# Kernel optimization log

Measured on AMD Instinct MI355X. Metric: run time of the kernel, lower is better.

Reference implementation:

```python
import jax, jax.numpy as jnp
import numpy as np

N_CLUSTERS = 2048
MAX_ITER = 5


def setup_inputs() -> dict:
    key = jax.random.key(0)
    k1, k2 = jax.random.split(key)
    X = jax.random.normal(k1, (131072, 128), dtype=jnp.float32)
    init_centroids = jax.random.normal(k2, (N_CLUSTERS, 128), dtype=jnp.float32)
    return {"X": X, "init_centroids": init_centroids}


def _euc_sim(a, b):
    # 2 a.b^T - |a|^2 - |b|^2  (negative squared euclidean distance)
    return (2.0 * (a @ b.T)
            - jnp.sum(a * a, axis=1)[:, None]
            - jnp.sum(b * b, axis=1)[None, :])


def reference(X, init_centroids):
    K = init_centroids.shape[0]

    def step(centroids, _):
        sim = _euc_sim(X, centroids)              # [N, K]
        closest = jnp.argmax(sim, axis=-1)         # [N]
        sums = jax.ops.segment_sum(X, closest, num_segments=K)        # [K, d]
        counts = jax.ops.segment_sum(jnp.ones_like(closest, dtype=X.dtype),
                                     closest, num_segments=K)         # [K]
        # full-batch branch: c_grad = mask @ x / mask.sum(-1), NaN -> 0
        c_grad = jnp.where(counts[:, None] > 0, sums / jnp.maximum(counts, 1.0)[:, None], 0.0)
        # minibatch is None => lr = 1 => centroids <- c_grad
        return c_grad, closest

    centroids, closest_hist = jax.lax.scan(step, init_centroids, None, length=MAX_ITER)
    labels = closest_hist[-1]
    return centroids, labels
```

## Files before the change

kernel.cpp:

```cpp
#include <hip/hip_runtime.h>
#include <hip/hip_bf16.h>

#define NP 131072
#define D 128
#define KC 2048
#define ITERS 5

#define TAU 0.03f

#if defined(__has_builtin)
#if __has_builtin(__builtin_amdgcn_global_load_lds)
#define USE_GLL 1
#endif
#endif

typedef short bf16x8 __attribute__((ext_vector_type(8)));
typedef float f32x4 __attribute__((ext_vector_type(4)));

__device__ inline unsigned short f2bf(float x) {
    __hip_bfloat16 b = __float2bfloat16(x);
    return *reinterpret_cast<unsigned short*>(&b);
}
__device__ inline float bf2f(unsigned short u) {
    union { unsigned int i; float f; } c; c.i = ((unsigned int)u) << 16; return c.f;
}

__device__ inline size_t pslot(int k, int d, int hl) {
    int g = k >> 4, t15 = k & 15, ks = d >> 5, q = (d >> 3) & 3, e = d & 7;
    return ((size_t)((ks * 128 + g) * 2 + hl)) * 512 + (q * 16 + t15) * 8 + e;
}

__global__ void init_kernel(const float* __restrict__ initC,
                            double* __restrict__ C64, double* __restrict__ CT64,
                            unsigned short* __restrict__ Pn) {
    int t = blockIdx.x * 256 + threadIdx.x;
    float v = initC[t];
    C64[t] = (double)v;
    CT64[(size_t)(t & 127) * KC + (t >> 7)] = (double)v;
    unsigned short h = f2bf(v);
    int k = t >> 7, d = t & 127;
    Pn[pslot(k, d, 0)] = h;
    Pn[pslot(k, d, 1)] = f2bf(v - bf2f(h));
}

__global__ void cnorm_kernel(const double* __restrict__ C64,
                             double* __restrict__ n64, float* __restrict__ n32,
                             int* __restrict__ counter) {
    int r = blockIdx.x * 4 + (threadIdx.x >> 6);
    int lane = threadIdx.x & 63;
    double a = C64[(size_t)r * D + lane * 2];
    double b = C64[(size_t)r * D + lane * 2 + 1];
    double s = a * a + b * b;
#pragma unroll
    for (int m = 1; m < 64; m <<= 1) s += __shfl_xor(s, m, 64);
    if (lane == 0) { n64[r] = s; n32[r] = (float)s; }
    if (blockIdx.x == 0 && threadIdx.x == 0) *counter = 0;
}

__global__ __launch_bounds__(256, 4)
void assign_kernel(const float* __restrict__ X,
                   const unsigned short* __restrict__ Pn,
                   const float* __restrict__ cnorm,
                   int* __restrict__ labels,
                   int* __restrict__ list,
                   int* __restrict__ counter) {
    __shared__ __align__(16) char lds[32768];

    const int tid = threadIdx.x;
    const int lane = tid & 63;
    const int wid = tid >> 6;
    const int wrow = wid >> 1;
    const int wcol = wid & 1;
    const int t15 = lane & 15;
    const int q = lane >> 4;
    const int pbase = blockIdx.x * 64;

#pragma unroll
    for (int i = 0; i < 8; i++) {
        int f = i * 256 + tid;
        int row = f >> 5, c4 = f & 31;
        float4 v = *(const float4*)&X[(size_t)(pbase + row) * D + c4 * 4];
        unsigned short h0 = f2bf(v.x), h1 = f2bf(v.y), h2 = f2bf(v.z), h3 = f2bf(v.w);
        unsigned short l0 = f2bf(v.x - bf2f(h0)), l1 = f2bf(v.y - bf2f(h1));
        unsigned short l2 = f2bf(v.z - bf2f(h2)), l3 = f2bf(v.w - bf2f(h3));
        uint2 ph = { (unsigned)h0 | ((unsigned)h1 << 16), (unsigned)h2 | ((unsigned)h3 << 16) };
        uint2 pl = { (unsigned)l0 | ((unsigned)l1 << 16), (unsigned)l2 | ((unsigned)l3 << 16) };
        int ad = (row * 256 + c4 * 8) ^ ((row & 7) << 4);
        *(uint2*)(lds + ad) = ph;
        *(uint2*)(lds + 16384 + ad) = pl;
    }
    __syncthreads();

    bf16x8 rah[2][4], ral[2][4];
#pragma unroll
    for (int rt = 0; rt < 2; rt++) {
        int row = wrow * 32 + rt * 16 + t15;
        int sw = (row & 7) << 4;
#pragma unroll
        for (int ks = 0; ks < 4; ks++) {
            int ad = (row * 256 + ks * 64 + q * 16) ^ sw;
            rah[rt][ks] = *(const bf16x8*)(lds + ad);
            ral[rt][ks] = *(const bf16x8*)(lds + 16384 + ad);
        }
    }
    __syncthreads();

    float b1[8], b2[8];
    int i1[8];
#pragma unroll
    for (int s = 0; s < 8; s++) { b1[s] = -INFINITY; b2[s] = -INFINITY; i1[s] = 0x7fffffff; }

    const char* PnB = (const char*)Pn;

#pragma unroll
    for (int i = 0; i < 4; i++) {
        int seg = wid * 4 + i;
        const char* src = PnB + seg * 1024;
#if USE_GLL
        __builtin_amdgcn_global_load_lds(
            (const __attribute__((address_space(1))) unsigned int*)(src + lane * 16),
            (__attribute__((address_space(3))) unsigned int*)(lds + seg * 1024),
            16, 0, 0);
#else
        uint4 v = *(const uint4*)(src + lane * 16);
        *(uint4*)(lds + seg * 1024 + lane * 16) = v;
#endif
    }
    __syncthreads();

    for (int ct = 0; ct < KC / 128; ct++) {
        f32x4 acc[2][4];
#pragma unroll
        for (int rt = 0; rt < 2; rt++)
#pragma unroll
            for (int cj = 0; cj < 4; cj++) acc[rt][cj] = (f32x4){0.f, 0.f, 0.f, 0.f};

#pragma unroll
        for (int ks = 0; ks < 4; ks++) {
            const int cur = (ct * 4 + ks) & 1;
            char* bcur = lds + cur * 16384;
            char* bnext = lds + (cur ^ 1) * 16384;

            const int nct = (ks == 3) ? ((ct < 15) ? ct + 1 : 15) : ct;
            const int nks = (ks + 1) & 3;
            const char* nsrc = PnB + ((size_t)(nks * 128 + nct * 8)) * 2048;
#pragma unroll
            for (int i = 0; i < 4; i++) {
                int seg = wid * 4 + i;
#if USE_GLL
                __builtin_amdgcn_global_load_lds(
                    (const __attribute__((address_space(1))) unsigned int*)(nsrc + seg * 1024 + lane * 16),
                    (__attribute__((address_space(3))) unsigned int*)(bnext + seg * 1024),
                    16, 0, 0);
#else
                uint4 v = *(const uint4*)(nsrc + seg * 1024 + lane * 16);
                *(uint4*)(bnext + seg * 1024 + lane * 16) = v;
#endif
            }

            __builtin_amdgcn_s_setprio(1);
#pragma unroll
            for (int cj = 0; cj < 4; cj++) {
                int gl = wcol * 4 + cj;
                bf16x8 bh = *(const bf16x8*)(bcur + gl * 2048 + lane * 16);
                bf16x8 bl = *(const bf16x8*)(bcur + gl * 2048 + 1024 + lane * 16);
#pragma unroll
                for (int rt = 0; rt < 2; rt++) {
                    acc[rt][cj] = __builtin_amdgcn_mfma_f32_16x16x32_bf16(rah[rt][ks], bh, acc[rt][cj], 0, 0, 0);
                    acc[rt][cj] = __builtin_amdgcn_mfma_f32_16x16x32_bf16(rah[rt][ks], bl, acc[rt][cj], 0, 0, 0);
                    acc[rt][cj] = __builtin_amdgcn_mfma_f32_16x16x32_bf16(ral[rt][ks], bh, acc[rt][cj], 0, 0, 0);
                }
            }
            __builtin_amdgcn_s_setprio(0);
            __syncthreads();
        }

#pragma unroll
        for (int cj = 0; cj < 4; cj++) {
            int col = ct * 128 + wcol * 64 + cj * 16 + t15;
            float cnv = cnorm[col];
#pragma unroll
            for (int rt = 0; rt < 2; rt++)
#pragma unroll
                for (int rg = 0; rg < 4; rg++) {
                    int s = rt * 4 + rg;
                    float sv = __builtin_fmaf(2.0f, acc[rt][cj][rg], -cnv);
                    bool gt1 = sv > b1[s];
                    float mx2 = fmaxf(b2[s], sv);
                    b2[s] = gt1 ? b1[s] : mx2;
                    i1[s] = gt1 ? col : i1[s];
                    b1[s] = gt1 ? sv : b1[s];
                }
        }
    }

#pragma unroll
    for (int s = 0; s < 8; s++) {
#pragma unroll
        for (int m = 1; m < 16; m <<= 1) {
            float ob1 = __shfl_xor(b1[s], m, 64);
            int   oi  = __shfl_xor(i1[s], m, 64);
            float ob2 = __shfl_xor(b2[s], m, 64);
            bool gt = ob1 > b1[s];
            bool eq = ob1 == b1[s];
            float nb2 = gt ? fmaxf(b1[s], ob2) : fmaxf(b2[s], ob1);
            nb2 = eq ? b1[s] : nb2;
            int ni = gt ? oi : i1[s];
            ni = (eq && oi < i1[s]) ? oi : ni;
            b1[s] = gt ? ob1 : b1[s];
            b2[s] = nb2;
            i1[s] = ni;
        }
    }

    __syncthreads();
    float* mb1 = (float*)lds;
    float* mb2 = ((float*)lds) + 128;
    int*   mi1 = (int*)(((float*)lds) + 256);
    if (t15 == 0) {
#pragma unroll
        for (int rt = 0; rt < 2; rt++)
#pragma unroll
            for (int rg = 0; rg < 4; rg++) {
                int s = rt * 4 + rg;
                int row = wrow * 32 + rt * 16 + q * 4 + rg;
                mb1[wcol * 64 + row] = b1[s];
                mb2[wcol * 64 + row] = b2[s];
                mi1[wcol * 64 + row] = i1[s];
            }
    }
    __syncthreads();
    if (tid < 64) {
        float a1 = mb1[tid], a2 = mb2[tid];  int ai = mi1[tid];
        float c1 = mb1[64 + tid], c2 = mb2[64 + tid];  int ci = mi1[64 + tid];
        float best, second;  int bi;
        if (a1 > c1)      { best = a1; bi = ai; second = fmaxf(a2, c1); }
        else if (a1 < c1) { best = c1; bi = ci; second = fmaxf(c2, a1); }
        else              { best = a1; bi = (ai < ci) ? ai : ci; second = a1; }
        int p = pbase + tid;
        labels[p] = bi;
        if (best - second < TAU) {
            int idx = atomicAdd(counter, 1);
            list[idx] = p;
        }
    }
}

__global__ void recheck_kernel(const float* __restrict__ X,
                               const double* __restrict__ CT64,
                               const double* __restrict__ cn64,
                               const int* __restrict__ list,
                               const int* __restrict__ counter,
                               int* __restrict__ labels) {
    __shared__ float xrow[D];
    __shared__ double rb[4];
    __shared__ int ri[4];
    int cnt = *counter;
    for (int ii = blockIdx.x; ii < cnt; ii += gridDim.x) {
        int p = list[ii];
        __syncthreads();
        if (threadIdx.x < D) xrow[threadIdx.x] = X[(size_t)p * D + threadIdx.x];
        __syncthreads();
        double xn = 0.0;
#pragma unroll 16
        for (int d = 0; d < D; d++) {
            double xv = (double)xrow[d];
            xn = fma(xv, xv, xn);
        }
        double best = -1.0e300;
        int bi = 0x7fffffff;
#pragma unroll
        for (int g = 0; g < 8; g++) {
            int c = threadIdx.x + 256 * g;
            double acc = 0.0;
#pragma unroll 16
            for (int d = 0; d < D; d++)
                acc = fma((double)xrow[d], CT64[(size_t)d * KC + c], acc);
            double s = 2.0 * acc - xn - cn64[c];
            if (s > best || (s == best && c < bi)) { best = s; bi = c; }
        }
#pragma unroll
        for (int m = 1; m < 64; m <<= 1) {
            double ob = __shfl_xor(best, m, 64);
            int oi = __shfl_xor(bi, m, 64);
            if (ob > best || (ob == best && oi < bi)) { best = ob; bi = oi; }
        }
        int w = threadIdx.x >> 6;
        if ((threadIdx.x & 63) == 0) { rb[w] = best; ri[w] = bi; }
        __syncthreads();
        if (threadIdx.x == 0) {
            double bb = rb[0]; int bbi = ri[0];
            for (int w2 = 1; w2 < 4; w2++)
                if (rb[w2] > bb || (rb[w2] == bb && ri[w2] < bbi)) { bb = rb[w2]; bbi = ri[w2]; }
            labels[p] = bbi;
        }
    }
}

__global__ void accum_kernel(const float* __restrict__ X,
                             const int* __restrict__ labels,
                             double* __restrict__ sums,
                             int* __restrict__ counts) {
    __shared__ double sred[4][D];
    __shared__ int cred[4];
    const int k = blockIdx.x;
    const int lane = threadIdx.x & 63;
    const int w = threadIdx.x >> 6;
    const int base0 = w * (NP / 4);
    double s0 = 0.0, s1 = 0.0;
    int cnt = 0;
    for (int it = 0; it < (NP / 4) / 256; it++) {
        int4 lab = *(const int4*)&labels[base0 + it * 256 + lane * 4];
#pragma unroll
        for (int j = 0; j < 4; j++) {
            int lv = (j == 0) ? lab.x : (j == 1) ? lab.y : (j == 2) ? lab.z : lab.w;
            unsigned long long m = __ballot(lv == k);
            cnt += __popcll(m);
            while (m) {
                int b = __ffsll(m) - 1;
                m &= m - 1;
                int p = base0 + it * 256 + b * 4 + j;
                float2 v = *(const float2*)&X[(size_t)p * D + lane * 2];
                s0 += (double)v.x;
                s1 += (double)v.y;
            }
        }
    }
    sred[w][lane * 2] = s0;
    sred[w][lane * 2 + 1] = s1;
    if (lane == 0) cred[w] = cnt;
    __syncthreads();
    if (threadIdx.x < D) {
        int d = threadIdx.x;
        double s = ((sred[0][d] + sred[1][d]) + sred[2][d]) + sred[3][d];
        sums[(size_t)k * D + d] = s;
    }
    if (threadIdx.x == 0)
        counts[k] = ((cred[0] + cred[1]) + cred[2]) + cred[3];
}

__global__ void update_kernel(const double* __restrict__ sums,
                              const int* __restrict__ counts,
                              double* __restrict__ C64, double* __restrict__ CT64,
                              unsigned short* __restrict__ Pn,
                              float* __restrict__ outC) {
    int t = blockIdx.x * 256 + threadIdx.x;
    int k = t >> 7;
    int n = counts[k];
    double v = (n > 0) ? sums[t] / (double)n : 0.0;
    C64[t] = v;
    CT64[(size_t)(t & 127) * KC + k] = v;
    float vf = (float)v;
    unsigned short h = f2bf(vf);
    int d = t & 127;
    Pn[pslot(k, d, 0)] = h;
    Pn[pslot(k, d, 1)] = f2bf(vf - bf2f(h));
    if (outC) outC[t] = vf;
}

__global__ void lab2f_kernel(const int* __restrict__ labels, float* __restrict__ out) {
    int t = blockIdx.x * 256 + threadIdx.x;
    out[t] = (float)labels[t];
}

extern "C" void kernel_launch(void* const* d_in, const int* in_sizes, int n_in,
                              void* d_out, int out_size, void* d_ws, size_t ws_size,
                              hipStream_t stream) {
    const float* X = (const float*)d_in[0];
    const float* initC = (const float*)d_in[1];
    float* out = (float*)d_out;

    char* w = (char*)d_ws;
    const size_t MB = 1u << 20;
    double* C64    = (double*)(w);
    double* S64    = (double*)(w + 2 * MB);
    double* CT64   = (double*)(w + 4 * MB);
    unsigned short* Pn = (unsigned short*)(w + 6 * MB);
    int*    labels = (int*)   (w + 7 * MB);
    int*    list   = (int*)   (w + 7 * MB + 512 * 1024);
    double* cn64   = (double*)(w + 8 * MB);
    float*  cn32   = (float*) (w + 8 * MB + 16 * 1024);
    int*    counts = (int*)   (w + 8 * MB + 24 * 1024);
    int*    counter= (int*)   (w + 8 * MB + 32 * 1024);

    init_kernel<<<(KC * D) / 256, 256, 0, stream>>>(initC, C64, CT64, Pn);

    for (int it = 0; it < ITERS; it++) {
        cnorm_kernel<<<KC / 4, 256, 0, stream>>>(C64, cn64, cn32, counter);
        assign_kernel<<<NP / 64, 256, 0, stream>>>(X, Pn, cn32, labels, list, counter);
        recheck_kernel<<<1024, 256, 0, stream>>>(X, CT64, cn64, list, counter, labels);
        accum_kernel<<<KC, 256, 0, stream>>>(X, labels, S64, counts);
        update_kernel<<<(KC * D) / 256, 256, 0, stream>>>(
            S64, counts, C64, CT64, Pn, (it == ITERS - 1) ? out : nullptr);
    }
    lab2f_kernel<<<NP / 256, 256, 0, stream>>>(labels, out + (size_t)KC * D);
}
```

Before: 2.169 ms.

## Replace per-cluster label scan with fixed-point atomic scatter accumulation

The accumulation kernel used to launch one block per cluster, and each block scanned all labels with ballots, so the whole label array was read 2048 times. It now launches one thread per point-dimension pair. Each thread converts its value to 64-bit fixed point and atomically adds it into the sum for its cluster, which keeps the result deterministic and order-independent. This adds two memsets per iteration and heavy 64-bit global atomic traffic with contention on popular clusters, and the fixed-point scale bounds both range and precision.

```diff
diff --git a/kernel.cpp b/kernel.cpp
--- a/kernel.cpp
+++ b/kernel.cpp
@@ -7,6 +7,7 @@
 #define ITERS 5
 
 #define TAU 0.03f
+#define FXS 274877906944.0
 
 #if defined(__has_builtin)
 #if __has_builtin(__builtin_amdgcn_global_load_lds)
@@ -299,47 +300,22 @@
 
 __global__ void accum_kernel(const float* __restrict__ X,
                              const int* __restrict__ labels,
-                             double* __restrict__ sums,
+                             unsigned long long* __restrict__ sumfx,
                              int* __restrict__ counts) {
-    __shared__ double sred[4][D];
-    __shared__ int cred[4];
-    const int k = blockIdx.x;
-    const int lane = threadIdx.x & 63;
-    const int w = threadIdx.x >> 6;
-    const int base0 = w * (NP / 4);
-    double s0 = 0.0, s1 = 0.0;
-    int cnt = 0;
-    for (int it = 0; it < (NP / 4) / 256; it++) {
-        int4 lab = *(const int4*)&labels[base0 + it * 256 + lane * 4];
-#pragma unroll
-        for (int j = 0; j < 4; j++) {
-            int lv = (j == 0) ? lab.x : (j == 1) ? lab.y : (j == 2) ? lab.z : lab.w;
-            unsigned long long m = __ballot(lv == k);
-            cnt += __popcll(m);
-            while (m) {
-                int b = __ffsll(m) - 1;
-                m &= m - 1;
-                int p = base0 + it * 256 + b * 4 + j;
-                float2 v = *(const float2*)&X[(size_t)p * D + lane * 2];
-                s0 += (double)v.x;
-                s1 += (double)v.y;
-            }
-        }
-    }
-    sred[w][lane * 2] = s0;
-    sred[w][lane * 2 + 1] = s1;
-    if (lane == 0) cred[w] = cnt;
-    __syncthreads();
-    if (threadIdx.x < D) {
-        int d = threadIdx.x;
-        double s = ((sred[0][d] + sred[1][d]) + sred[2][d]) + sred[3][d];
-        sums[(size_t)k * D + d] = s;
-    }
-    if (threadIdx.x == 0)
-        counts[k] = ((cred[0] + cred[1]) + cred[2]) + cred[3];
-}
-
-__global__ void update_kernel(const double* __restrict__ sums,
+    int t = blockIdx.x * 256 + threadIdx.x;
+    int p = t >> 6;
+    int lane = t & 63;
+    int lab = labels[p];
+    float2 v = *(const float2*)&X[(size_t)p * D + lane * 2];
+    long long fx = llrint((double)v.x * FXS);
+    long long fy = llrint((double)v.y * FXS);
+    unsigned long long* dst = &sumfx[(size_t)lab * D + lane * 2];
+    atomicAdd(&dst[0], (unsigned long long)fx);
+    atomicAdd(&dst[1], (unsigned long long)fy);
+    if (lane == 0) atomicAdd(&counts[lab], 1);
+}
+
+__global__ void update_kernel(const unsigned long long* __restrict__ sumfx,
                               const int* __restrict__ counts,
                               double* __restrict__ C64, double* __restrict__ CT64,
                               unsigned short* __restrict__ Pn,
@@ -347,7 +323,8 @@
     int t = blockIdx.x * 256 + threadIdx.x;
     int k = t >> 7;
     int n = counts[k];
-    double v = (n > 0) ? sums[t] / (double)n : 0.0;
+    double s = (double)(long long)sumfx[t] / FXS;
+    double v = (n > 0) ? s / (double)n : 0.0;
     C64[t] = v;
     CT64[(size_t)(t & 127) * KC + k] = v;
     float vf = (float)v;
@@ -373,7 +350,7 @@
     char* w = (char*)d_ws;
     const size_t MB = 1u << 20;
     double* C64    = (double*)(w);
-    double* S64    = (double*)(w + 2 * MB);
+    unsigned long long* sumfx = (unsigned long long*)(w + 2 * MB);
     double* CT64   = (double*)(w + 4 * MB);
     unsigned short* Pn = (unsigned short*)(w + 6 * MB);
     int*    labels = (int*)   (w + 7 * MB);
@@ -389,9 +366,11 @@
         cnorm_kernel<<<KC / 4, 256, 0, stream>>>(C64, cn64, cn32, counter);
         assign_kernel<<<NP / 64, 256, 0, stream>>>(X, Pn, cn32, labels, list, counter);
         recheck_kernel<<<1024, 256, 0, stream>>>(X, CT64, cn64, list, counter, labels);
-        accum_kernel<<<KC, 256, 0, stream>>>(X, labels, S64, counts);
+        hipMemsetAsync(sumfx, 0, (size_t)KC * D * sizeof(unsigned long long), stream);
+        hipMemsetAsync(counts, 0, KC * sizeof(int), stream);
+        accum_kernel<<<(NP * 64) / 256, 256, 0, stream>>>(X, labels, sumfx, counts);
         update_kernel<<<(KC * D) / 256, 256, 0, stream>>>(
-            S64, counts, C64, CT64, Pn, (it == ITERS - 1) ? out : nullptr);
+            sumfx, counts, C64, CT64, Pn, (it == ITERS - 1) ? out : nullptr);
     }
     lab2f_kernel<<<NP / 256, 256, 0, stream>>>(labels, out + (size_t)KC * D);
 }
```

After: 2.904 ms. 1.34x slower.

## Process eight clusters per block in accumulation to reuse label scans

Applied to the files above, without the earlier changes.

The accumulation kernel now assigns eight clusters to each block and uses 512 threads, instead of one cluster per 256-thread block. Each label read is tested against all eight clusters with ballots, which cuts redundant full scans of the label array by the group factor. The trade-off is more ballot work per label, more registers for the per-cluster double accumulators, and fewer blocks in flight.

```diff
diff --git a/kernel.cpp b/kernel.cpp
--- a/kernel.cpp
+++ b/kernel.cpp
@@ -5,6 +5,7 @@
 #define D 128
 #define KC 2048
 #define ITERS 5
+#define CG 8
 
 #define TAU 0.03f
 
@@ -297,46 +298,66 @@
     }
 }
 
-__global__ void accum_kernel(const float* __restrict__ X,
-                             const int* __restrict__ labels,
-                             double* __restrict__ sums,
-                             int* __restrict__ counts) {
-    __shared__ double sred[4][D];
-    __shared__ int cred[4];
-    const int k = blockIdx.x;
+__global__ __launch_bounds__(512)
+void accum_kernel(const float* __restrict__ X,
+                  const int* __restrict__ labels,
+                  double* __restrict__ sums,
+                  int* __restrict__ counts) {
+    __shared__ double sred[8][CG][64][2];
+    __shared__ int cred[8][CG];
     const int lane = threadIdx.x & 63;
     const int w = threadIdx.x >> 6;
-    const int base0 = w * (NP / 4);
-    double s0 = 0.0, s1 = 0.0;
-    int cnt = 0;
-    for (int it = 0; it < (NP / 4) / 256; it++) {
+    const int kbase = blockIdx.x * CG;
+    const int base0 = w * (NP / 8);
+    double s0[CG], s1[CG];
+    int cnt[CG];
+#pragma unroll
+    for (int c = 0; c < CG; c++) { s0[c] = 0.0; s1[c] = 0.0; cnt[c] = 0; }
+
+    for (int it = 0; it < (NP / 8) / 256; it++) {
         int4 lab = *(const int4*)&labels[base0 + it * 256 + lane * 4];
 #pragma unroll
         for (int j = 0; j < 4; j++) {
             int lv = (j == 0) ? lab.x : (j == 1) ? lab.y : (j == 2) ? lab.z : lab.w;
-            unsigned long long m = __ballot(lv == k);
-            cnt += __popcll(m);
-            while (m) {
-                int b = __ffsll(m) - 1;
-                m &= m - 1;
-                int p = base0 + it * 256 + b * 4 + j;
-                float2 v = *(const float2*)&X[(size_t)p * D + lane * 2];
-                s0 += (double)v.x;
-                s1 += (double)v.y;
+            int rel = lv - kbase;
+#pragma unroll
+            for (int c = 0; c < CG; c++) {
+                unsigned long long m = __ballot(rel == c);
+                cnt[c] += __popcll(m);
+                while (m) {
+                    int b = __ffsll(m) - 1;
+                    m &= m - 1;
+                    int p = base0 + it * 256 + b * 4 + j;
+                    float2 v = *(const float2*)&X[(size_t)p * D + lane * 2];
+                    s0[c] += (double)v.x;
+                    s1[c] += (double)v.y;
+                }
             }
         }
     }
-    sred[w][lane * 2] = s0;
-    sred[w][lane * 2 + 1] = s1;
-    if (lane == 0) cred[w] = cnt;
-    __syncthreads();
-    if (threadIdx.x < D) {
-        int d = threadIdx.x;
-        double s = ((sred[0][d] + sred[1][d]) + sred[2][d]) + sred[3][d];
-        sums[(size_t)k * D + d] = s;
-    }
-    if (threadIdx.x == 0)
-        counts[k] = ((cred[0] + cred[1]) + cred[2]) + cred[3];
+#pragma unroll
+    for (int c = 0; c < CG; c++) {
+        sred[w][c][lane][0] = s0[c];
+        sred[w][c][lane][1] = s1[c];
+    }
+    if (lane < CG) cred[w][lane] = cnt[lane];
+    __syncthreads();
+
+#pragma unroll
+    for (int rep = 0; rep < 2; rep++) {
+        int idx = rep * 512 + threadIdx.x;
+        int c = idx >> 7, d = idx & 127;
+        double s = 0.0;
+#pragma unroll
+        for (int ww = 0; ww < 8; ww++) s += sred[ww][c][d >> 1][d & 1];
+        sums[(size_t)(kbase + c) * D + d] = s;
+    }
+    if (threadIdx.x < CG) {
+        int s = 0;
+#pragma unroll
+        for (int ww = 0; ww < 8; ww++) s += cred[ww][threadIdx.x];
+        counts[kbase + threadIdx.x] = s;
+    }
 }
 
 __global__ void update_kernel(const double* __restrict__ sums,
@@ -389,7 +410,7 @@
         cnorm_kernel<<<KC / 4, 256, 0, stream>>>(C64, cn64, cn32, counter);
         assign_kernel<<<NP / 64, 256, 0, stream>>>(X, Pn, cn32, labels, list, counter);
         recheck_kernel<<<1024, 256, 0, stream>>>(X, CT64, cn64, list, counter, labels);
-        accum_kernel<<<KC, 256, 0, stream>>>(X, labels, S64, counts);
+        accum_kernel<<<KC / CG, 512, 0, stream>>>(X, labels, S64, counts);
         update_kernel<<<(KC * D) / 256, 256, 0, stream>>>(
             S64, counts, C64, CT64, Pn, (it == ITERS - 1) ? out : nullptr);
     }
```

Result: slower. 2.247 ms (+3.6%).
